# Performance work log

Measured on AMD Instinct MI355X. Metric: run time of the kernel, lower is better.

The kernel has to match this reference:

```python
import jax, jax.numpy as jnp
import numpy as np

T, B, D, K = 256, 128, 1024, 21
PAD = 0


def setup_inputs() -> dict:
    key = jax.random.key(0)
    k1, k2, k3, k4, k5, k6, k7 = jax.random.split(key, 7)
    lstm_features = jax.random.normal(k1, (T, B, D), dtype=jnp.float32)
    # gold tags: non-pad (1..K-1) for a random prefix, PAD afterwards; mask[0] all on
    tags = jax.random.randint(k2, (T, B), 1, K)
    lengths = jax.random.randint(k3, (B,), T // 2, T + 1)
    tags = jnp.where(jnp.arange(T)[:, None] < lengths[None, :], tags, PAD)
    W = jax.random.normal(k4, (D, K), dtype=jnp.float32) * 0.02
    b = jnp.zeros((K,), dtype=jnp.float32)
    # torchcrf initializes transitions uniform(-0.1, 0.1)
    start_transitions = jax.random.uniform(k5, (K,), minval=-0.1, maxval=0.1)
    end_transitions = jax.random.uniform(k6, (K,), minval=-0.1, maxval=0.1)
    transitions = jax.random.uniform(k7, (K, K), minval=-0.1, maxval=0.1)
    return {
        'lstm_features': lstm_features,
        'tags': tags,
        'W': W,
        'b': b,
        'start_transitions': start_transitions,
        'end_transitions': end_transitions,
        'transitions': transitions,
    }


def _crf_nll(emissions, tags, mask, start, end, trans):
    # emissions: (T,B,K), tags/mask: (T,B). Returns -sum_b log p(tags|emissions)
    maskf = mask.astype(emissions.dtype)
    # --- numerator: score of gold path (fully vectorized over t) ---
    em_score = jnp.take_along_axis(emissions, tags[:, :, None], axis=2)[:, :, 0]  # (T,B)
    tr_score = trans[tags[:-1], tags[1:]]                                          # (T-1,B)
    num = start[tags[0]] + em_score[0]
    num = num + jnp.sum((tr_score + em_score[1:]) * maskf[1:], axis=0)
    seq_ends = jnp.sum(mask.astype(jnp.int32), axis=0) - 1                         # (B,)
    last_tags = jnp.take_along_axis(tags, seq_ends[None, :], axis=0)[0]
    num = num + end[last_tags]
    # --- denominator: forward algorithm (log partition) via scan ---
    def step(score, xs):  # score: (B,K)
        emit_t, mask_t = xs
        nxt = jax.nn.logsumexp(score[:, :, None] + trans[None, :, :] + emit_t[:, None, :], axis=1)
        return jnp.where(mask_t[:, None], nxt, score), None
    score0 = start[None, :] + emissions[0]
    scoreT, _ = jax.lax.scan(step, score0, (emissions[1:], mask[1:]))
    den = jax.nn.logsumexp(scoreT + end[None, :], axis=1)                          # (B,)
    return -jnp.sum(num - den)


def _viterbi(emissions, mask, start, end, trans):
    # returns best tag sequence (T,B) int32, padded positions set to PAD
    n_tags = emissions.shape[-1]
    ident = jnp.arange(n_tags, dtype=jnp.int32)[None, :]
    def step(score, xs):  # score: (B,K)
        emit_t, mask_t = xs
        cand = score[:, :, None] + trans[None, :, :]          # (B, prev K, next K)
        best_prev = jnp.argmax(cand, axis=1).astype(jnp.int32)  # (B,K)
        nxt = jnp.max(cand, axis=1) + emit_t
        ptr = jnp.where(mask_t[:, None], best_prev, ident)    # identity ptr on padding
        new_score = jnp.where(mask_t[:, None], nxt, score)
        return new_score, ptr
    score0 = start[None, :] + emissions[0]
    scoreT, history = jax.lax.scan(step, score0, (emissions[1:], mask[1:]))  # history: (T-1,B,K)
    last_tag = jnp.argmax(scoreT + end[None, :], axis=1).astype(jnp.int32)   # (B,)
    def back(tag, hist_t):
        prev = jnp.take_along_axis(hist_t, tag[:, None], axis=1)[:, 0]
        return prev, tag
    first_tag, rest = jax.lax.scan(back, last_tag, history, reverse=True)    # rest = tags[1:]
    best = jnp.concatenate([first_tag[None, :], rest], axis=0)               # (T,B)
    return jnp.where(mask, best, PAD)


def reference(lstm_features, tags, W, b, start_transitions, end_transitions, transitions):
    # Linear projection; dropout is identity at inference
    fc_out = jnp.einsum('tbd,dk->tbk', lstm_features, W) + b
    mask = tags != PAD
    crf_out = _viterbi(fc_out, mask, start_transitions, end_transitions, transitions)
    crf_loss = _crf_nll(fc_out, tags, mask, start_transitions, end_transitions, transitions)
    return crf_out, crf_loss
```

## Files before the change

kernel.cpp:

```cpp
#include <hip/hip_runtime.h>
#include <math.h>

#define T_ 256
#define B_ 128
#define D_ 1024
#define K_ 21
#define NB3 43

typedef short v8s __attribute__((ext_vector_type(8)));
typedef float v4f __attribute__((ext_vector_type(4)));

__device__ __forceinline__ short bf16rne(float f) {
  unsigned u = __float_as_uint(f);
  u += 0x7FFFu + ((u >> 16) & 1u);
  return (short)(u >> 16);
}
__device__ __forceinline__ float rdl(float v, int l) {
  return __int_as_float(__builtin_amdgcn_readlane(__float_as_int(v), l));
}

__global__ __launch_bounds__(256) void fc_kernel(
    const float* __restrict__ A, const float* __restrict__ W,
    const float* __restrict__ bias, float* __restrict__ fc) {
  __shared__ float red[3][64][22];
  const int lane = threadIdx.x & 63;
  const int wv = threadIdx.x >> 6;
  const int m15 = lane & 15, g4 = lane >> 4;
  const int rowbase = blockIdx.x * 64;
  const int kc = wv * 256;
  const int n1 = 16 + m15;

  v8s bf[8][2];
#pragma unroll
  for (int s = 0; s < 8; ++s) {
    const float* Wp = W + (size_t)(kc + 32 * s + 8 * g4) * K_;
#pragma unroll
    for (int j = 0; j < 8; ++j) bf[s][0][j] = bf16rne(Wp[j * K_ + m15]);
    if (n1 < K_) {
#pragma unroll
      for (int j = 0; j < 8; ++j) bf[s][1][j] = bf16rne(Wp[j * K_ + n1]);
    } else {
#pragma unroll
      for (int j = 0; j < 8; ++j) bf[s][1][j] = 0;
    }
  }

  v4f acc[4][2];
#pragma unroll
  for (int m = 0; m < 4; ++m) {
    acc[m][0] = (v4f)(0.f);
    acc[m][1] = (v4f)(0.f);
  }

#pragma unroll
  for (int s = 0; s < 8; ++s) {
    v8s av[4];
#pragma unroll
    for (int m = 0; m < 4; ++m) {
      const float* Ap =
          A + (size_t)(rowbase + 16 * m + m15) * D_ + kc + 32 * s + 8 * g4;
      const float4 x = *(const float4*)Ap;
      const float4 y = *(const float4*)(Ap + 4);
      av[m][0] = bf16rne(x.x); av[m][1] = bf16rne(x.y);
      av[m][2] = bf16rne(x.z); av[m][3] = bf16rne(x.w);
      av[m][4] = bf16rne(y.x); av[m][5] = bf16rne(y.y);
      av[m][6] = bf16rne(y.z); av[m][7] = bf16rne(y.w);
    }
#pragma unroll
    for (int m = 0; m < 4; ++m) {
      acc[m][0] = __builtin_amdgcn_mfma_f32_16x16x32_bf16(av[m], bf[s][0],
                                                          acc[m][0], 0, 0, 0);
      acc[m][1] = __builtin_amdgcn_mfma_f32_16x16x32_bf16(av[m], bf[s][1],
                                                          acc[m][1], 0, 0, 0);
    }
  }

  if (wv > 0) {
#pragma unroll
    for (int m = 0; m < 4; ++m)
#pragma unroll
      for (int ri = 0; ri < 4; ++ri) {
        const int rl = 16 * m + 4 * g4 + ri;
        red[wv - 1][rl][m15] = acc[m][0][ri];
        if (n1 < K_) red[wv - 1][rl][n1] = acc[m][1][ri];
      }
  }
  __syncthreads();
  if (wv == 0) {
    const float b0 = bias[m15];
    const float b1 = (n1 < K_) ? bias[n1] : 0.f;
#pragma unroll
    for (int m = 0; m < 4; ++m)
#pragma unroll
      for (int ri = 0; ri < 4; ++ri) {
        const int rl = 16 * m + 4 * g4 + ri;
        float* o = fc + (size_t)(rowbase + rl) * K_;
        o[m15] = acc[m][0][ri] + red[0][rl][m15] + red[1][rl][m15] +
                 red[2][rl][m15] + b0;
        if (n1 < K_)
          o[n1] = acc[m][1][ri] + red[0][rl][n1] + red[1][rl][n1] +
                  red[2][rl][n1] + b1;
      }
  }
}

__global__ __launch_bounds__(64) void scan_kernel(
    const float* __restrict__ fc, const int* __restrict__ tags,
    const float* __restrict__ startT, const float* __restrict__ endT,
    const float* __restrict__ trans, float* __restrict__ out_tags,
    float* __restrict__ out_loss) {
  __shared__ unsigned short bp[256 * 66];
  __shared__ unsigned char h2[127 * 66];
  __shared__ unsigned char h4[63 * 66];
  __shared__ unsigned char cur[3 * 256];
  __shared__ v4f statev[18];

  const int lane = threadIdx.x;
  const int blk = blockIdx.x;

  if (blk < 2 * NB3) {
    const bool fwd = blk < NB3;
    const int bblk = fwd ? blk : blk - NB3;
    int g = lane / 21;
    if (g > 2) g = 2;
    int jloc = lane - g * 21;
    if (jloc > 20) jloc = 20;
    int batch = bblk * 3 + g;
    if (batch >= B_) batch = B_ - 1;

    int len0 = 0, len1 = 0, len2 = 0;
#pragma unroll
    for (int q = 0; q < 4; ++q) {
      const int t = q * 64 + lane;
      int b0 = bblk * 3, b1 = bblk * 3 + 1, b2 = bblk * 3 + 2;
      if (b1 >= B_) b1 = B_ - 1;
      if (b2 >= B_) b2 = B_ - 1;
      len0 += __popcll(__ballot(tags[t * B_ + b0] != 0));
      len1 += __popcll(__ballot(tags[t * B_ + b1] != 0));
      len2 += __popcll(__ballot(tags[t * B_ + b2] != 0));
    }
    const int mylen = (g == 0) ? len0 : (g == 1) ? len1 : len2;

    float* sb = (float*)statev + g * 24;
    const v4f* sv = (const v4f*)sb;

#define FCAT(t) fc[((size_t)(t) * B_ + batch) * K_ + jloc]
    const float em0 = FCAT(0);

    if (fwd) {
      float ec[21];
#pragma unroll
      for (int i = 0; i < K_; ++i) ec[i] = __expf(trans[i * K_ + jloc]);
      float p = __expf(startT[jloc] + em0);
      sb[jloc] = p;
      float L = 0.f;
      float sA = FCAT(2), sB = FCAT(3), sC = FCAT(4), sD = FCAT(5);
      float ee = __expf(FCAT(1));

#define FWD_STEP(t, RA, RB, RC, RD)                                          \
      {                                                                      \
        const v4f A0 = sv[0], A1 = sv[1], A2 = sv[2], A3 = sv[3],            \
                  A4 = sv[4];                                                \
        const float A5 = sb[20];                                             \
        const float eet = ee;                                                \
        ee = __expf(RA);               \
        {                                                                    \
          const int tn = ((t) + 5 < T_) ? (t) + 5 : T_ - 1;                  \
          RA = FCAT(tn);                           \
        }                                                                    \
        float d0 = A0[0] * ec[0], d1 = A0[1] * ec[1], d2 = A0[2] * ec[2];    \
        d0 = fmaf(A0[3], ec[3], d0); d1 = fmaf(A1[0], ec[4], d1);            \
        d2 = fmaf(A1[1], ec[5], d2);                                         \
        d0 = fmaf(A1[2], ec[6], d0); d1 = fmaf(A1[3], ec[7], d1);            \
        d2 = fmaf(A2[0], ec[8], d2);                                         \
        d0 = fmaf(A2[1], ec[9], d0); d1 = fmaf(A2[2], ec[10], d1);           \
        d2 = fmaf(A2[3], ec[11], d2);                                        \
        d0 = fmaf(A3[0], ec[12], d0); d1 = fmaf(A3[1], ec[13], d1);          \
        d2 = fmaf(A3[2], ec[14], d2);                                        \
        d0 = fmaf(A3[3], ec[15], d0); d1 = fmaf(A4[0], ec[16], d1);          \
        d2 = fmaf(A4[1], ec[17], d2);                                        \
        d0 = fmaf(A4[2], ec[18], d0); d1 = fmaf(A4[3], ec[19], d1);          \
        d2 = fmaf(A5, ec[20], d2);                                           \
        const float pn = ((d0 + d1) + d2) * eet;                             \
        p = ((t) < mylen) ? pn : p;                                          \
        if (((t) & 7) == 0) {                                                \
                        \
          const float f = A0[0];                                             \
          p *= __builtin_amdgcn_rcpf(f);                                     \
          L += __logf(f);                                                    \
        }                                                                    \
        sb[jloc] = p;                                \
      }

      for (int t = 1; t + 3 <= 252; t += 4) {
        FWD_STEP(t + 0, sA, sB, sC, sD)
        FWD_STEP(t + 1, sB, sC, sD, sA)
        FWD_STEP(t + 2, sC, sD, sA, sB)
        FWD_STEP(t + 3, sD, sA, sB, sC)
      }
      FWD_STEP(253, sA, sB, sC, sD)
      FWD_STEP(254, sB, sC, sD, sA)
      FWD_STEP(255, sC, sD, sA, sB)
#undef FWD_STEP

      const float w = p * __expf(endT[jloc]);
      float res = 0.f;
#pragma unroll
      for (int gg = 0; gg < 3; ++gg) {
        if (bblk * 3 + gg < B_) {
          float tot = 0.f;
#pragma unroll
          for (int i = 0; i < K_; ++i) tot += rdl(w, gg * K_ + i);
          res += rdl(L, gg * K_) + __logf(tot);
        }
      }
      if (lane == 0) atomicAdd(out_loss, res);
    } else {
      float tr[21];
#pragma unroll
      for (int i = 0; i < K_; ++i) tr[i] = trans[i * K_ + jloc] + 2048.0f;
      float sc = startT[jloc] + em0;
      sb[jloc] = sc;
      float sA = FCAT(1), sB = FCAT(2), sC = FCAT(3), sD = FCAT(4);

#define VIT_STEP(t, RA, RB, RC, RD)                                          \
      {                                                                      \
        const v4f A0 = sv[0], A1 = sv[1], A2 = sv[2], A3 = sv[3],            \
                  A4 = sv[4];                                                \
        const float A5 = sb[20];                                             \
        const float emt = RA;                 \
        {                                                                    \
          const int tn = ((t) + 4 < T_) ? (t) + 4 : T_ - 1;                  \
          RA = FCAT(tn);                                                     \
        }                                                                    \
        int k0 = 0, k1 = 0, k2 = 0;      \
           \
        const float c0 = A0[0] + tr[0];                                      \
        k0 = (__float_as_int(c0) & 0xFFFFFFE0) | 20;                         \
        const float c1 = A0[1] + tr[1];                                      \
        k1 = (__float_as_int(c1) & 0xFFFFFFE0) | 19;                         \
        const float c2 = A0[2] + tr[2];                                      \
        k2 = (__float_as_int(c2) & 0xFFFFFFE0) | 18;                         \
        {                                                                    \
          const float c = A0[3] + tr[3];                                     \
          const int kk = (__float_as_int(c) & 0xFFFFFFE0) | 17;              \
          k0 = k0 > kk ? k0 : kk;                                            \
        }                                                                    \
        {                                                                    \
          const float c = A1[0] + tr[4];                                     \
          const int kk = (__float_as_int(c) & 0xFFFFFFE0) | 16;              \
          k1 = k1 > kk ? k1 : kk;                                            \
        }                                                                    \
        {                                                                    \
          const float c = A1[1] + tr[5];                                     \
          const int kk = (__float_as_int(c) & 0xFFFFFFE0) | 15;              \
          k2 = k2 > kk ? k2 : kk;                                            \
        }                                                                    \
        {                                                                    \
          const float c = A1[2] + tr[6];                                     \
          const int kk = (__float_as_int(c) & 0xFFFFFFE0) | 14;              \
          k0 = k0 > kk ? k0 : kk;                                            \
        }                                                                    \
        {                                                                    \
          const float c = A1[3] + tr[7];                                     \
          const int kk = (__float_as_int(c) & 0xFFFFFFE0) | 13;              \
          k1 = k1 > kk ? k1 : kk;                                            \
        }                                                                    \
        {                                                                    \
          const float c = A2[0] + tr[8];                                     \
          const int kk = (__float_as_int(c) & 0xFFFFFFE0) | 12;              \
          k2 = k2 > kk ? k2 : kk;                                            \
        }                                                                    \
        {                                                                    \
          const float c = A2[1] + tr[9];                                     \
          const int kk = (__float_as_int(c) & 0xFFFFFFE0) | 11;              \
          k0 = k0 > kk ? k0 : kk;                                            \
        }                                                                    \
        {                                                                    \
          const float c = A2[2] + tr[10];                                    \
          const int kk = (__float_as_int(c) & 0xFFFFFFE0) | 10;              \
          k1 = k1 > kk ? k1 : kk;                                            \
        }                                                                    \
        {                                                                    \
          const float c = A2[3] + tr[11];                                    \
          const int kk = (__float_as_int(c) & 0xFFFFFFE0) | 9;               \
          k2 = k2 > kk ? k2 : kk;                                            \
        }                                                                    \
        {                                                                    \
          const float c = A3[0] + tr[12];                                    \
          const int kk = (__float_as_int(c) & 0xFFFFFFE0) | 8;               \
          k0 = k0 > kk ? k0 : kk;                                            \
        }                                                                    \
        {                                                                    \
          const float c = A3[1] + tr[13];                                    \
          const int kk = (__float_as_int(c) & 0xFFFFFFE0) | 7;               \
          k1 = k1 > kk ? k1 : kk;                                            \
        }                                                                    \
        {                                                                    \
          const float c = A3[2] + tr[14];                                    \
          const int kk = (__float_as_int(c) & 0xFFFFFFE0) | 6;               \
          k2 = k2 > kk ? k2 : kk;                                            \
        }                                                                    \
        {                                                                    \
          const float c = A3[3] + tr[15];                                    \
          const int kk = (__float_as_int(c) & 0xFFFFFFE0) | 5;               \
          k0 = k0 > kk ? k0 : kk;                                            \
        }                                                                    \
        {                                                                    \
          const float c = A4[0] + tr[16];                                    \
          const int kk = (__float_as_int(c) & 0xFFFFFFE0) | 4;               \
          k1 = k1 > kk ? k1 : kk;                                            \
        }                                                                    \
        {                                                                    \
          const float c = A4[1] + tr[17];                                    \
          const int kk = (__float_as_int(c) & 0xFFFFFFE0) | 3;               \
          k2 = k2 > kk ? k2 : kk;                                            \
        }                                                                    \
        {                                                                    \
          const float c = A4[2] + tr[18];                                    \
          const int kk = (__float_as_int(c) & 0xFFFFFFE0) | 2;               \
          k0 = k0 > kk ? k0 : kk;                                            \
        }                                                                    \
        {                                                                    \
          const float c = A4[3] + tr[19];                                    \
          const int kk = (__float_as_int(c) & 0xFFFFFFE0) | 1;               \
          k1 = k1 > kk ? k1 : kk;                                            \
        }                                                                    \
        {                                                                    \
          const float c = A5 + tr[20];                                       \
          const int kk = (__float_as_int(c) & 0xFFFFFFE0) | 0;               \
          k2 = k2 > kk ? k2 : kk;                                            \
        }                                                                    \
        int km = k0 > k1 ? k0 : k1;                                          \
        km = km > k2 ? km : k2;                                              \
        const float nxt = __int_as_float(km & 0xFFFFFFE0) - 2048.0f + emt;   \
        const bool m = (t) < mylen;                                          \
        sc = m ? nxt : sc;                                                   \
        sb[jloc] = sc;                               \
        const int pw = m ? (20 - (km & 31)) : jloc;                          \
        if (lane < 63) bp[(t) * 66 + g * 22 + jloc] = (unsigned short)pw;    \
      }

      for (int t = 1; t + 3 <= 252; t += 4) {
        VIT_STEP(t + 0, sA, sB, sC, sD)
        VIT_STEP(t + 1, sB, sC, sD, sA)
        VIT_STEP(t + 2, sC, sD, sA, sB)
        VIT_STEP(t + 3, sD, sA, sB, sC)
      }
      VIT_STEP(253, sA, sB, sC, sD)
      VIT_STEP(254, sB, sC, sD, sA)
      VIT_STEP(255, sC, sD, sA, sB)
#undef VIT_STEP
      __syncthreads();

      const float finb = sc + endT[jloc] + 2048.0f;
      const int myk = (__float_as_int(finb) & 0xFFFFFFE0) | (20 - jloc);
      int last0 = 0, last1 = 0, last2 = 0;
#pragma unroll
      for (int gg = 0; gg < 3; ++gg) {
        int km = 0;
#pragma unroll
        for (int i = 0; i < K_; ++i) {
          const int ki = __builtin_amdgcn_readlane(myk, gg * K_ + i);
          km = km > ki ? km : ki;
        }
        const int lt = 20 - (km & 31);
        if (gg == 0) last0 = lt;
        else if (gg == 1) last1 = lt;
        else last2 = lt;
      }

      for (int i = lane; i < 127 * 63; i += 64) {
        const int v = i / 63;
        const int rem = i - v * 63;
        const int gg = rem / 21, j = rem - (rem / 21) * 21;
        h2[v * 66 + gg * 22 + j] = (unsigned char)
            bp[(2 * v + 1) * 66 + gg * 22 + bp[(2 * v + 2) * 66 + gg * 22 + j]];
      }
      __syncthreads();
      for (int i = lane; i < 63 * 63; i += 64) {
        const int w = i / 63;
        const int rem = i - w * 63;
        const int gg = rem / 21, j = rem - (rem / 21) * 21;
        h4[w * 66 + gg * 22 + j] =
            h2[(2 * w) * 66 + gg * 22 + h2[(2 * w + 1) * 66 + gg * 22 + j]];
      }
      __syncthreads();

      if (lane < 3 && bblk * 3 + lane < B_) {
        int c = (lane == 0) ? last0 : (lane == 1) ? last1 : last2;
        cur[lane * 256 + 255] = (unsigned char)c;
        c = bp[255 * 66 + lane * 22 + c];
        cur[lane * 256 + 254] = (unsigned char)c;
        c = h2[126 * 66 + lane * 22 + c];
        cur[lane * 256 + 252] = (unsigned char)c;
        for (int w = 62; w >= 0; --w) {
          c = h4[w * 66 + lane * 22 + c];
          cur[lane * 256 + 4 * w] = (unsigned char)c;
        }
      }
      __syncthreads();
      for (int i = lane; i < 63 * 3; i += 64) {
        const int gg = i / 63, ii = i - (i / 63) * 63;
        const int t = 2 + 4 * ii;
        cur[gg * 256 + t] =
            h2[(t >> 1) * 66 + gg * 22 + cur[gg * 256 + t + 2]];
      }
      __syncthreads();
      for (int i = lane; i < 127 * 3; i += 64) {
        const int gg = i / 127, ii = i - (i / 127) * 127;
        const int t = 1 + 2 * ii;
        cur[gg * 256 + t] = (unsigned char)
            bp[(t + 1) * 66 + gg * 22 + cur[gg * 256 + t + 1]];
      }
      __syncthreads();
      for (int i = lane; i < 3 * 256; i += 64) {
        const int gg = i >> 8, t = i & 255;
        const int bb = bblk * 3 + gg;
        const int lg = (gg == 0) ? len0 : (gg == 1) ? len1 : len2;
        if (bb < B_)
          out_tags[t * B_ + bb] = (t < lg) ? (float)cur[gg * 256 + t] : 0.f;
      }
    }
#undef FCAT
  } else {
    const int b = blk - 2 * NB3;
    float contrib = 0.f;
#pragma unroll
    for (int q = 0; q < 4; ++q) {
      const int t = lane * 4 + q;
      const int tg = tags[t * B_ + b];
      const size_t ro = ((size_t)t * B_ + b) * K_;
      if (t == 0) {
        contrib += startT[tg] + fc[ro + tg];
      } else if (tg != 0) {
        const int pg = tags[(t - 1) * B_ + b];
        contrib += trans[pg * K_ + tg] + fc[ro + tg];
      }
      const bool isLast =
          (tg != 0) && (t == T_ - 1 || tags[(t + 1) * B_ + b] == 0);
      if (isLast) contrib += endT[tg];
    }
#pragma unroll
    for (int off = 32; off > 0; off >>= 1)
      contrib += __shfl_down(contrib, off, 64);
    if (lane == 0) atomicAdd(out_loss, -contrib);
  }
}

extern "C" void kernel_launch(void* const* d_in, const int* in_sizes, int n_in,
                              void* d_out, int out_size, void* d_ws,
                              size_t ws_size, hipStream_t stream) {
  const float* A = (const float*)d_in[0];
  const int* tags = (const int*)d_in[1];
  const float* W = (const float*)d_in[2];
  const float* bias = (const float*)d_in[3];
  const float* startT = (const float*)d_in[4];
  const float* endT = (const float*)d_in[5];
  const float* trans = (const float*)d_in[6];

  float* out_tags = (float*)d_out;
  float* out_loss = (float*)d_out + (size_t)T_ * B_;
  float* fc = (float*)d_ws;

  hipMemsetAsync(out_loss, 0, sizeof(float), stream);
  fc_kernel<<<512, 256, 0, stream>>>(A, W, bias, fc);
  scan_kernel<<<2 * NB3 + B_, 64, 0, stream>>>(fc, tags, startT, endT, trans,
                                               out_tags, out_loss);
}
```

Before: 277.8 us.

## Fold loss zeroing into fc kernel, rescale less often, tree-reduce Viterbi max

The separate memset launch is replaced by having block 0 of fc_kernel zero the loss accumulator, which removes one launch from the stream. The forward-algorithm renormalisation now runs every 16 steps instead of every 8, cutting rcp and log work at some risk of float overflow or underflow in the unnormalised probabilities. The Viterbi max over 21 packed keys is restructured as a balanced tree of 3-way maxes, which shortens the dependency chain and may map to a 3-input max instruction. The lane<63 guard on the backpointer store is removed, so lane 63 now also writes its value.

```diff
diff --git a/kernel.cpp b/kernel.cpp
--- a/kernel.cpp
+++ b/kernel.cpp
@@ -18,11 +18,17 @@
 __device__ __forceinline__ float rdl(float v, int l) {
   return __int_as_float(__builtin_amdgcn_readlane(__float_as_int(v), l));
 }
+__device__ __forceinline__ int imax3(int a, int b, int c) {
+  const int t = a > b ? a : b;
+  return t > c ? t : c;
+}
 
 __global__ __launch_bounds__(256) void fc_kernel(
     const float* __restrict__ A, const float* __restrict__ W,
-    const float* __restrict__ bias, float* __restrict__ fc) {
+    const float* __restrict__ bias, float* __restrict__ fc,
+    float* __restrict__ out_loss) {
   __shared__ float red[3][64][22];
+  if (blockIdx.x == 0 && threadIdx.x == 0) *out_loss = 0.f;
   const int lane = threadIdx.x & 63;
   const int wv = threadIdx.x >> 6;
   const int m15 = lane & 15, g4 = lane >> 4;
@@ -183,8 +189,9 @@
         d2 = fmaf(A5, ec[20], d2);                                           \
         const float pn = ((d0 + d1) + d2) * eet;                             \
         p = ((t) < mylen) ? pn : p;                                          \
-        if (((t) & 7) == 0) {                                                \
-                        \
+        if (((t) & 15) == 0) {                                               \
+            \
+            \
           const float f = A0[0];                                             \
           p *= __builtin_amdgcn_rcpf(f);                                     \
           L += __logf(f);                                                    \
@@ -223,6 +230,7 @@
       sb[jloc] = sc;
       float sA = FCAT(1), sB = FCAT(2), sC = FCAT(3), sD = FCAT(4);
 
+#define KEY(i, V) ((__float_as_int((V) + tr[i]) & 0xFFFFFFE0) | (20 - (i)))
 #define VIT_STEP(t, RA, RB, RC, RD)                                          \
       {                                                                      \
         const v4f A0 = sv[0], A1 = sv[1], A2 = sv[2], A3 = sv[3],            \
@@ -233,112 +241,22 @@
           const int tn = ((t) + 4 < T_) ? (t) + 4 : T_ - 1;                  \
           RA = FCAT(tn);                                                     \
         }                                                                    \
-        int k0 = 0, k1 = 0, k2 = 0;      \
-           \
-        const float c0 = A0[0] + tr[0];                                      \
-        k0 = (__float_as_int(c0) & 0xFFFFFFE0) | 20;                         \
-        const float c1 = A0[1] + tr[1];                                      \
-        k1 = (__float_as_int(c1) & 0xFFFFFFE0) | 19;                         \
-        const float c2 = A0[2] + tr[2];                                      \
-        k2 = (__float_as_int(c2) & 0xFFFFFFE0) | 18;                         \
-        {                                                                    \
-          const float c = A0[3] + tr[3];                                     \
-          const int kk = (__float_as_int(c) & 0xFFFFFFE0) | 17;              \
-          k0 = k0 > kk ? k0 : kk;                                            \
-        }                                                                    \
-        {                                                                    \
-          const float c = A1[0] + tr[4];                                     \
-          const int kk = (__float_as_int(c) & 0xFFFFFFE0) | 16;              \
-          k1 = k1 > kk ? k1 : kk;                                            \
-        }                                                                    \
-        {                                                                    \
-          const float c = A1[1] + tr[5];                                     \
-          const int kk = (__float_as_int(c) & 0xFFFFFFE0) | 15;              \
-          k2 = k2 > kk ? k2 : kk;                                            \
-        }                                                                    \
-        {                                                                    \
-          const float c = A1[2] + tr[6];                                     \
-          const int kk = (__float_as_int(c) & 0xFFFFFFE0) | 14;              \
-          k0 = k0 > kk ? k0 : kk;                                            \
-        }                                                                    \
-        {                                                                    \
-          const float c = A1[3] + tr[7];                                     \
-          const int kk = (__float_as_int(c) & 0xFFFFFFE0) | 13;              \
-          k1 = k1 > kk ? k1 : kk;                                            \
-        }                                                                    \
-        {                                                                    \
-          const float c = A2[0] + tr[8];                                     \
-          const int kk = (__float_as_int(c) & 0xFFFFFFE0) | 12;              \
-          k2 = k2 > kk ? k2 : kk;                                            \
-        }                                                                    \
-        {                                                                    \
-          const float c = A2[1] + tr[9];                                     \
-          const int kk = (__float_as_int(c) & 0xFFFFFFE0) | 11;              \
-          k0 = k0 > kk ? k0 : kk;                                            \
-        }                                                                    \
-        {                                                                    \
-          const float c = A2[2] + tr[10];                                    \
-          const int kk = (__float_as_int(c) & 0xFFFFFFE0) | 10;              \
-          k1 = k1 > kk ? k1 : kk;                                            \
-        }                                                                    \
-        {                                                                    \
-          const float c = A2[3] + tr[11];                                    \
-          const int kk = (__float_as_int(c) & 0xFFFFFFE0) | 9;               \
-          k2 = k2 > kk ? k2 : kk;                                            \
-        }                                                                    \
-        {                                                                    \
-          const float c = A3[0] + tr[12];                                    \
-          const int kk = (__float_as_int(c) & 0xFFFFFFE0) | 8;               \
-          k0 = k0 > kk ? k0 : kk;                                            \
-        }                                                                    \
-        {                                                                    \
-          const float c = A3[1] + tr[13];                                    \
-          const int kk = (__float_as_int(c) & 0xFFFFFFE0) | 7;               \
-          k1 = k1 > kk ? k1 : kk;                                            \
-        }                                                                    \
-        {                                                                    \
-          const float c = A3[2] + tr[14];                                    \
-          const int kk = (__float_as_int(c) & 0xFFFFFFE0) | 6;               \
-          k2 = k2 > kk ? k2 : kk;                                            \
-        }                                                                    \
-        {                                                                    \
-          const float c = A3[3] + tr[15];                                    \
-          const int kk = (__float_as_int(c) & 0xFFFFFFE0) | 5;               \
-          k0 = k0 > kk ? k0 : kk;                                            \
-        }                                                                    \
-        {                                                                    \
-          const float c = A4[0] + tr[16];                                    \
-          const int kk = (__float_as_int(c) & 0xFFFFFFE0) | 4;               \
-          k1 = k1 > kk ? k1 : kk;                                            \
-        }                                                                    \
-        {                                                                    \
-          const float c = A4[1] + tr[17];                                    \
-          const int kk = (__float_as_int(c) & 0xFFFFFFE0) | 3;               \
-          k2 = k2 > kk ? k2 : kk;                                            \
-        }                                                                    \
-        {                                                                    \
-          const float c = A4[2] + tr[18];                                    \
-          const int kk = (__float_as_int(c) & 0xFFFFFFE0) | 2;               \
-          k0 = k0 > kk ? k0 : kk;                                            \
-        }                                                                    \
-        {                                                                    \
-          const float c = A4[3] + tr[19];                                    \
-          const int kk = (__float_as_int(c) & 0xFFFFFFE0) | 1;               \
-          k1 = k1 > kk ? k1 : kk;                                            \
-        }                                                                    \
-        {                                                                    \
-          const float c = A5 + tr[20];                                       \
-          const int kk = (__float_as_int(c) & 0xFFFFFFE0) | 0;               \
-          k2 = k2 > kk ? k2 : kk;                                            \
-        }                                                                    \
-        int km = k0 > k1 ? k0 : k1;                                          \
-        km = km > k2 ? km : k2;                                              \
+        const int q0 = imax3(KEY(0, A0[0]), KEY(1, A0[1]), KEY(2, A0[2]));   \
+        const int q1 = imax3(KEY(3, A0[3]), KEY(4, A1[0]), KEY(5, A1[1]));   \
+        const int q2 = imax3(KEY(6, A1[2]), KEY(7, A1[3]), KEY(8, A2[0]));   \
+        const int q3 = imax3(KEY(9, A2[1]), KEY(10, A2[2]), KEY(11, A2[3])); \
+        const int q4 = imax3(KEY(12, A3[0]), KEY(13, A3[1]),                 \
+                             KEY(14, A3[2]));                                \
+        const int q5 = imax3(KEY(15, A3[3]), KEY(16, A4[0]),                 \
+                             KEY(17, A4[1]));                                \
+        const int q6 = imax3(KEY(18, A4[2]), KEY(19, A4[3]), KEY(20, A5));   \
+        const int km = imax3(imax3(q0, q1, q2), imax3(q3, q4, q5), q6);      \
         const float nxt = __int_as_float(km & 0xFFFFFFE0) - 2048.0f + emt;   \
         const bool m = (t) < mylen;                                          \
         sc = m ? nxt : sc;                                                   \
         sb[jloc] = sc;                               \
         const int pw = m ? (20 - (km & 31)) : jloc;                          \
-        if (lane < 63) bp[(t) * 66 + g * 22 + jloc] = (unsigned short)pw;    \
+        bp[(t) * 66 + g * 22 + jloc] = (unsigned short)pw;                   \
       }
 
       for (int t = 1; t + 3 <= 252; t += 4) {
@@ -351,6 +269,7 @@
       VIT_STEP(254, sB, sC, sD, sA)
       VIT_STEP(255, sC, sD, sA, sB)
 #undef VIT_STEP
+#undef KEY
       __syncthreads();
 
       const float finb = sc + endT[jloc] + 2048.0f;
@@ -379,11 +298,11 @@
       }
       __syncthreads();
       for (int i = lane; i < 63 * 63; i += 64) {
-        const int w = i / 63;
-        const int rem = i - w * 63;
+        const int w2 = i / 63;
+        const int rem = i - w2 * 63;
         const int gg = rem / 21, j = rem - (rem / 21) * 21;
-        h4[w * 66 + gg * 22 + j] =
-            h2[(2 * w) * 66 + gg * 22 + h2[(2 * w + 1) * 66 + gg * 22 + j]];
+        h4[w2 * 66 + gg * 22 + j] =
+            h2[(2 * w2) * 66 + gg * 22 + h2[(2 * w2 + 1) * 66 + gg * 22 + j]];
       }
       __syncthreads();
 
@@ -394,9 +313,9 @@
         cur[lane * 256 + 254] = (unsigned char)c;
         c = h2[126 * 66 + lane * 22 + c];
         cur[lane * 256 + 252] = (unsigned char)c;
-        for (int w = 62; w >= 0; --w) {
-          c = h4[w * 66 + lane * 22 + c];
-          cur[lane * 256 + 4 * w] = (unsigned char)c;
+        for (int w2 = 62; w2 >= 0; --w2) {
+          c = h4[w2 * 66 + lane * 22 + c];
+          cur[lane * 256 + 4 * w2] = (unsigned char)c;
         }
       }
       __syncthreads();
@@ -463,8 +382,7 @@
   float* out_loss = (float*)d_out + (size_t)T_ * B_;
   float* fc = (float*)d_ws;
 
-  hipMemsetAsync(out_loss, 0, sizeof(float), stream);
-  fc_kernel<<<512, 256, 0, stream>>>(A, W, bias, fc);
+  fc_kernel<<<512, 256, 0, stream>>>(A, W, bias, fc, out_loss);
   scan_kernel<<<2 * NB3 + B_, 64, 0, stream>>>(fc, tags, startT, endT, trans,
                                                out_tags, out_loss);
 }
```

Result: no change. 273.5 us (-1.6%).
